# Optimization experiments

Hardware: AMD Instinct MI355X
Metric: run time of the kernel (lower is better)

Reference implementation:

```python
import jax, jax.numpy as jnp
import numpy as np

B, N, DIM = 2, 4096, 1024
QK = 128
HID = 2048  # int(2.0 * DIM)
EPS = 1e-5


def setup_inputs() -> dict:
    key = jax.random.key(0)
    ks = jax.random.split(key, 10)
    s = lambda fan_in: 1.0 / np.sqrt(fan_in)
    return {
        "x": jax.random.normal(ks[0], (B, N, DIM), dtype=jnp.float32),
        "ln_g": jnp.ones((DIM,), jnp.float32),
        "ln_b": jnp.zeros((DIM,), jnp.float32),
        "Wh": jax.random.uniform(ks[1], (DIM, 2 * HID), jnp.float32, -s(DIM), s(DIM)),
        "bh": jax.random.uniform(ks[2], (2 * HID,), jnp.float32, -s(DIM), s(DIM)),
        "Wqk": jax.random.uniform(ks[3], (DIM, QK), jnp.float32, -s(DIM), s(DIM)),
        "bqk": jax.random.uniform(ks[4], (QK,), jnp.float32, -s(DIM), s(DIM)),
        "gamma": 1.0 + 0.02 * jax.random.normal(ks[5], (2, QK), jnp.float32),
        "beta": jnp.zeros((2, QK), jnp.float32),
        "Wo": jax.random.uniform(ks[6], (HID, DIM), jnp.float32, -s(HID), s(HID)),
        "bo": jax.random.uniform(ks[7], (DIM,), jnp.float32, -s(HID), s(HID)),
    }


def _gau(x, ln_g, ln_b, Wh, bh, Wqk, bqk, gamma, beta, Wo, bo):
    n = x.shape[-2]
    # LayerNorm
    mu = jnp.mean(x, axis=-1, keepdims=True)
    var = jnp.var(x, axis=-1, keepdims=True)
    normed = (x - mu) * jax.lax.rsqrt(var + EPS) * ln_g + ln_b
    # hidden: v and gate
    hv = jax.nn.silu(normed @ Wh + bh)           # [b, n, 2*HID]
    v, gate = hv[..., :HID], hv[..., HID:]
    # q, k via shared projection + offset-scale (2 heads)
    qk = jax.nn.silu(normed @ Wqk + bqk)         # [b, n, QK]
    q = qk * gamma[0] + beta[0]
    k = qk * gamma[1] + beta[1]
    # ReLU^2 attention, scaled by 1/seq_len
    sim = jnp.einsum('bid,bjd->bij', q, k) / n   # [b, n, n]
    attn = jnp.square(jax.nn.relu(sim))
    # causal mask (zero out strict upper triangle)
    causal = jnp.tril(jnp.ones((n, n), dtype=bool))
    attn = jnp.where(causal, attn, 0.0)
    out = jnp.einsum('bij,bjd->bid', attn, v) * gate
    out = out @ Wo + bo
    return out + x  # residual


def reference(x, ln_g, ln_b, Wh, bh, Wqk, bqk, gamma, beta, Wo, bo):
    return _gau(x, ln_g, ln_b, Wh, bh, Wqk, bqk, gamma, beta, Wo, bo)
```

## Files before the change

kernel.cpp:

```cpp
#include <hip/hip_runtime.h>
#include <math.h>

typedef unsigned short u16;
typedef unsigned int u32;
typedef __attribute__((ext_vector_type(8))) __bf16 bf16x8;
typedef __attribute__((ext_vector_type(4))) float f32x4;

#define B_ 2
#define N_ 4096
#define DIM_ 1024
#define QK_ 128
#define HID_ 2048
#define M_TOT (B_*N_)

__device__ __forceinline__ u16 f2bf(float f) {
  union { float f; u32 u; } v; v.f = f;
  u32 r = v.u + 0x7fffu + ((v.u >> 16) & 1u);
  return (u16)(r >> 16);
}
__device__ __forceinline__ float bf2f(u16 h) {
  union { u32 u; float f; } v; v.u = ((u32)h) << 16;
  return v.f;
}
__device__ __forceinline__ float silu_f(float v) { return v / (1.0f + expf(-v)); }

#define WAIT_VM(n)  asm volatile("s_waitcnt vmcnt(" #n ")" ::: "memory")

__global__ __launch_bounds__(256) void ln_kernel(
    const float* __restrict__ x, const float* __restrict__ g,
    const float* __restrict__ b, u16* __restrict__ out) {
  const int row = blockIdx.x;
  const int t = threadIdx.x;
  const float4* xr = (const float4*)(x + (size_t)row * DIM_);
  float4 v = xr[t];
  float s  = v.x + v.y + v.z + v.w;
  float s2 = v.x*v.x + v.y*v.y + v.z*v.z + v.w*v.w;
  #pragma unroll
  for (int o = 32; o > 0; o >>= 1) { s += __shfl_down(s, o); s2 += __shfl_down(s2, o); }
  __shared__ float red[2][4];
  const int wave = t >> 6, lane = t & 63;
  if (lane == 0) { red[0][wave] = s; red[1][wave] = s2; }
  __syncthreads();
  float ts  = red[0][0] + red[0][1] + red[0][2] + red[0][3];
  float ts2 = red[1][0] + red[1][1] + red[1][2] + red[1][3];
  float mu  = ts * (1.0f/(float)DIM_);
  float var = ts2 * (1.0f/(float)DIM_) - mu*mu;
  float rs  = rsqrtf(var + 1e-5f);
  const float4 gg = ((const float4*)g)[t];
  const float4 bb = ((const float4*)b)[t];
  ushort4 w;
  w.x = f2bf((v.x-mu)*rs*gg.x + bb.x);
  w.y = f2bf((v.y-mu)*rs*gg.y + bb.y);
  w.z = f2bf((v.z-mu)*rs*gg.z + bb.z);
  w.w = f2bf((v.w-mu)*rs*gg.w + bb.w);
  ((ushort4*)(out + (size_t)row*DIM_))[t] = w;
}

__global__ __launch_bounds__(256) void transpose_k(
    const float* __restrict__ in, u16* __restrict__ out, int R, int C) {
  __shared__ float tile[32][33];
  const int c0 = blockIdx.x * 32, r0 = blockIdx.y * 32;
  const int tx = threadIdx.x & 31, ty = threadIdx.x >> 5;
  #pragma unroll
  for (int i = 0; i < 4; ++i)
    tile[ty + i*8][tx] = in[(size_t)(r0 + ty + i*8) * C + c0 + tx];
  __syncthreads();
  #pragma unroll
  for (int i = 0; i < 4; ++i)
    out[(size_t)(c0 + ty + i*8) * R + r0 + tx] = f2bf(tile[tx][ty + i*8]);
}

enum { EPI_HV, EPI_QK, EPI_S, EPI_PV, EPI_O };

template<int EPI>
__global__ __launch_bounds__(256, 4) void g2(
    const u16* __restrict__ A, int lda,
    const u16* __restrict__ BT, int ldb, int K,
    void* __restrict__ Cv, int ldc,
    const float* __restrict__ f0,
    const u16* __restrict__ gateT, const float* __restrict__ xres)
{
  int bm, bn; const int bz = blockIdx.z;
  if constexpr (EPI == EPI_HV) {
    const int id  = (int)blockIdx.x + 32*(int)blockIdx.y;
    const int nid = (id & 7)*256 + (id >> 3);
    bm = nid & 31; bn = nid >> 5;
  } else if constexpr (EPI == EPI_O) {
    const int id  = (int)blockIdx.x + 64*(int)blockIdx.y;
    const int nid = (id & 7)*64 + (id >> 3);
    bm = nid & 63; bn = nid >> 6;
  } else if constexpr (EPI == EPI_PV) {
    bn = blockIdx.x;
    bm = bz ? ((int)gridDim.y - 1 - (int)blockIdx.y) : (int)blockIdx.y;
  } else {
    bn = blockIdx.x; bm = blockIdx.y;
    if (bm < bn) return;
  }

  const u16* Ap = A; const u16* Bp = BT;
  if constexpr (EPI == EPI_S)  { Ap += (size_t)bz*N_*QK_; Bp += (size_t)bz*N_*QK_; }
  if constexpr (EPI == EPI_PV) { Ap += (size_t)bz*N_*N_;  Bp += (size_t)bz*N_; }

  __shared__ __align__(16) u16 lds[2][128*64];
  const int tid = threadIdx.x, wave = tid >> 6, lane = tid & 63;
  const int m0 = bm*128, n0 = bn*128;
  int kmax = K;
  if constexpr (EPI == EPI_PV) kmax = (bm+1)*128;
  f32x4 acc[4][4] = {};
  const int wr = (wave >> 1)*64, wc = (wave & 1)*64;

  const int srow = lane >> 3;
  const int sch  = (lane & 7) ^ srow;
  const u16* ga = Ap + (size_t)(m0 + srow)*lda + sch*8;
  const u16* gb = Bp + (size_t)(n0 + srow)*ldb + sch*8;

  const int l15   = lane & 15;
  const int cswz0 = ((((lane>>4)    ) ^ (lane&7)) << 3);
  const int cswz1 = ((((lane>>4) | 4) ^ (lane&7)) << 3);

  for (int k0 = 0; k0 < kmax; k0 += 64) {
    #pragma unroll
    for (int t = 0; t < 4; ++t) {
      const int chunk = wave*4 + t;
      __builtin_amdgcn_global_load_lds(
          (const __attribute__((address_space(1))) void*)(ga + (size_t)(chunk*8)*lda + k0),
          (__attribute__((address_space(3))) void*)&lds[0][chunk*512], 16, 0, 0);
      __builtin_amdgcn_global_load_lds(
          (const __attribute__((address_space(1))) void*)(gb + (size_t)(chunk*8)*ldb + k0),
          (__attribute__((address_space(3))) void*)&lds[1][chunk*512], 16, 0, 0);
    }
    __syncthreads();
    #pragma unroll
    for (int kk = 0; kk < 2; ++kk) {
      const int cs = kk ? cswz1 : cswz0;
      bf16x8 af[4], bfr[4];
      #pragma unroll
      for (int i = 0; i < 4; ++i) {
        af[i]  = *(const bf16x8*)&lds[0][(wr + i*16 + l15)*64 + cs];
        bfr[i] = *(const bf16x8*)&lds[1][(wc + i*16 + l15)*64 + cs];
      }
      #pragma unroll
      for (int i = 0; i < 4; ++i)
        #pragma unroll
        for (int j = 0; j < 4; ++j)
          acc[i][j] = __builtin_amdgcn_mfma_f32_16x16x32_bf16(af[i], bfr[j], acc[i][j], 0, 0, 0);
    }
    __syncthreads();
  }

  const int er = (lane >> 4)*4;
  #pragma unroll
  for (int i = 0; i < 4; ++i) {
    #pragma unroll
    for (int j = 0; j < 4; ++j) {
      #pragma unroll
      for (int e = 0; e < 4; ++e) {
        const int row = m0 + wr + i*16 + er + e;
        const int col = n0 + wc + j*16 + l15;
        float v = acc[i][j][e];
        if constexpr (EPI == EPI_HV) {
          ((u16*)Cv)[(size_t)row*ldc + col] = f2bf(silu_f(v + f0[row]));
        } else if constexpr (EPI == EPI_S) {
          float p = (row >= col && v > 0.0f) ? v*v : 0.0f;
          ((u16*)Cv)[(size_t)bz*N_*N_ + (size_t)row*ldc + col] = f2bf(p);
        } else if constexpr (EPI == EPI_PV) {
          float gate = bf2f(gateT[(size_t)(HID_ + col)*M_TOT + (size_t)bz*N_ + row]);
          ((u16*)Cv)[((size_t)bz*N_ + row)*ldc + col] = f2bf(v * gate);
        } else {
          ((float*)Cv)[(size_t)row*ldc + col] = v + f0[col] + xres[(size_t)row*DIM_ + col];
        }
      }
    }
  }
}

template<int BM, int EPI>
__global__ __launch_bounds__(256, 2) void ring4(
    const u16* __restrict__ A, int lda,
    const u16* __restrict__ BT, int ldb, int K,
    void* __restrict__ Cv, void* __restrict__ C2v, int ldc,
    const float* __restrict__ f0, const float* __restrict__ f1,
    const float* __restrict__ f2)
{
  constexpr int FRM  = BM/32;
  constexpr int LA   = BM/64;
  constexpr int ASZ  = BM*32;
  constexpr int SLOT = ASZ + 128*32;
  __shared__ __align__(16) u16 lds[4*SLOT];

  const int bm = blockIdx.x, bn = blockIdx.y;
  const int tid = threadIdx.x, wave = tid >> 6, lane = tid & 63;
  const int wm = wave >> 1, wn = wave & 1;
  const int m0 = bm*BM, n0 = bn*128;
  const int nt = K >> 5;

  f32x4 acc[FRM][4] = {};
  const int srow = lane >> 2;
  const int sq   = (lane & 3) ^ ((srow >> 1) & 3);

  auto stage = [&](int t) {
    if (t >= nt) return;
    const int k0 = t << 5;
    u16* sA = &lds[(t & 3) * SLOT];
    u16* sB = sA + ASZ;
    #pragma unroll
    for (int c = 0; c < LA; ++c) {
      const int ch = wave*LA + c;
      const u16* src = A + (size_t)(m0 + ch*16 + srow)*lda + k0 + sq*8;
      __builtin_amdgcn_global_load_lds(
          (const __attribute__((address_space(1))) void*)src,
          (__attribute__((address_space(3))) void*)(sA + ch*512), 16, 0, 0);
    }
    #pragma unroll
    for (int c = 0; c < 2; ++c) {
      const int ch = wave*2 + c;
      const u16* src = BT + (size_t)(n0 + ch*16 + srow)*ldb + k0 + sq*8;
      __builtin_amdgcn_global_load_lds(
          (const __attribute__((address_space(1))) void*)src,
          (__attribute__((address_space(3))) void*)(sB + ch*512), 16, 0, 0);
    }
  };

  stage(0); stage(1); stage(2);

  const int l15 = lane & 15;
  const int swz = (((lane >> 4) ^ ((l15 >> 1) & 3)) << 3);
  const int rA0 = (wm*(BM/2) + l15)*32;
  const int rB0 = (wn*64 + l15)*32;

  for (int t = 0; t < nt; ++t) {
    if (t + 2 < nt)      { WAIT_VM(8); }
    else if (t + 1 < nt) { WAIT_VM(4); }
    else                 { WAIT_VM(0); }
    __builtin_amdgcn_s_barrier();
    stage(t + 3);

    const u16* sA = &lds[(t & 3) * SLOT];
    const u16* sB = sA + ASZ;
    bf16x8 a_[FRM], b_[4];
    #pragma unroll
    for (int j = 0; j < 4; ++j) b_[j] = *(const bf16x8*)&sB[rB0 + j*512 + swz];
    #pragma unroll
    for (int i = 0; i < FRM; ++i) a_[i] = *(const bf16x8*)&sA[rA0 + i*512 + swz];
    #pragma unroll
    for (int i = 0; i < FRM; ++i)
      #pragma unroll
      for (int j = 0; j < 4; ++j)
        acc[i][j] = __builtin_amdgcn_mfma_f32_16x16x32_bf16(a_[i], b_[j], acc[i][j], 0, 0, 0);
  }

  const int er = (lane >> 4)*4;
  #pragma unroll
  for (int fi = 0; fi < FRM; ++fi) {
    #pragma unroll
    for (int fj = 0; fj < 4; ++fj) {
      #pragma unroll
      for (int e = 0; e < 4; ++e) {
        const int row = m0 + wm*(BM/2) + fi*16 + er + e;
        const int col = n0 + wn*64 + fj*16 + l15;
        float v = acc[fi][fj][e];
        if constexpr (EPI == EPI_QK) {
          float s = silu_f(v + f0[col]);
          float q = (s*f1[col]     + f2[col])     * (1.0f/(float)N_);
          float k2 = s*f1[QK_+col] + f2[QK_+col];
          ((u16*)Cv )[(size_t)row*ldc + col] = f2bf(q);
          ((u16*)C2v)[(size_t)row*ldc + col] = f2bf(k2);
        }
      }
    }
  }
}

extern "C" void kernel_launch(void* const* d_in, const int* in_sizes, int n_in,
                              void* d_out, int out_size, void* d_ws, size_t ws_size,
                              hipStream_t stream) {
  const float* x    = (const float*)d_in[0];
  const float* ln_g = (const float*)d_in[1];
  const float* ln_b = (const float*)d_in[2];
  const float* Wh   = (const float*)d_in[3];
  const float* bh   = (const float*)d_in[4];
  const float* Wqk  = (const float*)d_in[5];
  const float* bqk  = (const float*)d_in[6];
  const float* gamma= (const float*)d_in[7];
  const float* beta = (const float*)d_in[8];
  const float* Wo   = (const float*)d_in[9];
  const float* bo   = (const float*)d_in[10];
  float* out = (float*)d_out;
  char* ws = (char*)d_ws;

  u16* normed = (u16*)(ws + 0);
  u16* WhT    = (u16*)(ws + 16777216);
  u16* WqkT   = (u16*)(ws + 25165824);
  u16* WoT    = (u16*)(ws + 25427968);
  u16* hvT    = (u16*)(ws + 29622272);
  u16* qs     = (u16*)(ws + 96731136);
  u16* kb     = (u16*)(ws + 98828288);
  u16* P      = (u16*)(ws + 100925440);
  u16* a2     = (u16*)(ws + 168034304);

  ln_kernel<<<M_TOT, 256, 0, stream>>>(x, ln_g, ln_b, normed);
  transpose_k<<<dim3(4096/32, 1024/32), 256, 0, stream>>>(Wh,  WhT,  1024, 4096);
  transpose_k<<<dim3( 128/32, 1024/32), 256, 0, stream>>>(Wqk, WqkT, 1024, 128);
  transpose_k<<<dim3(1024/32, 2048/32), 256, 0, stream>>>(Wo,  WoT,  2048, 1024);

  g2<EPI_HV><<<dim3(32, 64), 256, 0, stream>>>(WhT, 1024, normed, 1024, 1024,
      hvT, 8192, bh, nullptr, nullptr);
  ring4<64, EPI_QK><<<dim3(128, 1), 256, 0, stream>>>(normed, 1024, WqkT, 1024, 1024,
      qs, kb, 128, bqk, gamma, beta);
  g2<EPI_S><<<dim3(32, 32, 2), 256, 0, stream>>>(qs, 128, kb, 128, 128,
      P, 4096, nullptr, nullptr, nullptr);
  g2<EPI_PV><<<dim3(16, 32, 2), 256, 0, stream>>>(P, 4096, hvT, 8192, 4096,
      a2, 2048, nullptr, hvT, nullptr);
  g2<EPI_O><<<dim3(64, 8), 256, 0, stream>>>(a2, 2048, WoT, 2048, 2048,
      out, 1024, bo, nullptr, x);
}
```

Before: 284.6 us.

## Add 8-wave ping-pong pipelined GEMM kernel for HV, PV and output projections

```diff
diff --git a/kernel.cpp b/kernel.cpp
--- a/kernel.cpp
+++ b/kernel.cpp
@@ -25,6 +25,7 @@
 __device__ __forceinline__ float silu_f(float v) { return v / (1.0f + expf(-v)); }
 
 #define WAIT_VM(n)  asm volatile("s_waitcnt vmcnt(" #n ")" ::: "memory")
+#define WAIT_LG0()  asm volatile("s_waitcnt lgkmcnt(0)" ::: "memory")
 
 __global__ __launch_bounds__(256) void ln_kernel(
     const float* __restrict__ x, const float* __restrict__ g,
@@ -81,31 +82,15 @@
     const u16* __restrict__ gateT, const float* __restrict__ xres)
 {
   int bm, bn; const int bz = blockIdx.z;
-  if constexpr (EPI == EPI_HV) {
-    const int id  = (int)blockIdx.x + 32*(int)blockIdx.y;
-    const int nid = (id & 7)*256 + (id >> 3);
-    bm = nid & 31; bn = nid >> 5;
-  } else if constexpr (EPI == EPI_O) {
-    const int id  = (int)blockIdx.x + 64*(int)blockIdx.y;
-    const int nid = (id & 7)*64 + (id >> 3);
-    bm = nid & 63; bn = nid >> 6;
-  } else if constexpr (EPI == EPI_PV) {
-    bn = blockIdx.x;
-    bm = bz ? ((int)gridDim.y - 1 - (int)blockIdx.y) : (int)blockIdx.y;
-  } else {
-    bn = blockIdx.x; bm = blockIdx.y;
-    if (bm < bn) return;
-  }
+  bn = blockIdx.x; bm = blockIdx.y;
+  if constexpr (EPI == EPI_S) { if (bm < bn) return; }
 
   const u16* Ap = A; const u16* Bp = BT;
   if constexpr (EPI == EPI_S)  { Ap += (size_t)bz*N_*QK_; Bp += (size_t)bz*N_*QK_; }
-  if constexpr (EPI == EPI_PV) { Ap += (size_t)bz*N_*N_;  Bp += (size_t)bz*N_; }
 
   __shared__ __align__(16) u16 lds[2][128*64];
   const int tid = threadIdx.x, wave = tid >> 6, lane = tid & 63;
   const int m0 = bm*128, n0 = bn*128;
-  int kmax = K;
-  if constexpr (EPI == EPI_PV) kmax = (bm+1)*128;
   f32x4 acc[4][4] = {};
   const int wr = (wave >> 1)*64, wc = (wave & 1)*64;
 
@@ -118,7 +103,7 @@
   const int cswz0 = ((((lane>>4)    ) ^ (lane&7)) << 3);
   const int cswz1 = ((((lane>>4) | 4) ^ (lane&7)) << 3);
 
-  for (int k0 = 0; k0 < kmax; k0 += 64) {
+  for (int k0 = 0; k0 < K; k0 += 64) {
     #pragma unroll
     for (int t = 0; t < 4; ++t) {
       const int chunk = wave*4 + t;
@@ -158,11 +143,162 @@
         const int row = m0 + wr + i*16 + er + e;
         const int col = n0 + wc + j*16 + l15;
         float v = acc[i][j][e];
+        if constexpr (EPI == EPI_S) {
+          float p = (row >= col && v > 0.0f) ? v*v : 0.0f;
+          ((u16*)Cv)[(size_t)bz*N_*N_ + (size_t)row*ldc + col] = f2bf(p);
+        }
+      }
+    }
+  }
+}
+
+template<int BM, int EPI>
+__global__ __launch_bounds__(512, 2) void p8(
+    const u16* __restrict__ A, int lda,
+    const u16* __restrict__ BT, int ldb, int K,
+    void* __restrict__ Cv, int ldc,
+    const float* __restrict__ f0,
+    const u16* __restrict__ gateT, const float* __restrict__ xres)
+{
+  constexpr int FR  = BM/32;
+  constexpr int HF  = FR/2;
+  constexpr int ATL = BM*64;
+  constexpr int SLT = ATL + 256*64;
+  __shared__ __align__(16) u16 lds[2*SLT];
+
+  int bm, bn;
+  const int bz = blockIdx.z;
+  if constexpr (EPI == EPI_HV) {
+    const int id  = (int)blockIdx.x + 16*(int)blockIdx.y;
+    const int nid = (id & 7)*64 + (id >> 3);
+    bm = nid & 15; bn = nid >> 4;
+  } else if constexpr (EPI == EPI_PV) {
+    bn = blockIdx.x;
+    bm = bz ? ((int)gridDim.y - 1 - (int)blockIdx.y) : (int)blockIdx.y;
+  } else { bm = blockIdx.x; bn = blockIdx.y; }
+
+  const int tid = threadIdx.x, wave = tid >> 6, lane = tid & 63;
+  const int wm = wave >> 2, wn = wave & 3;
+  const int m0 = bm*BM, n0 = bn*256;
+  const u16* Ap = A; const u16* Bp = BT;
+  if constexpr (EPI == EPI_PV) { Ap += (size_t)bz*N_*N_; Bp += (size_t)bz*N_; }
+  int kmax = K;
+  if constexpr (EPI == EPI_PV) kmax = (bm+1)*BM;
+  const int nt = kmax >> 6;
+
+  const int l15  = lane & 15;
+  const int c0   = (((lane>>4)    ) ^ (lane&7)) << 3;
+  const int c1   = (((lane>>4) | 4) ^ (lane&7)) << 3;
+  const int srow = lane >> 3;
+  const int scol = ((lane&7) ^ (lane>>3)) << 3;
+
+  f32x4 acc[FR][4] = {};
+  bf16x8 af[HF][2], b0[2][2], b1[2][2];
+
+  auto stage = [&](int slot, int unit, int t) {
+    if (t >= nt) return;
+    const int k0 = t << 6;
+    if (unit == 0 || unit == 3) {
+      const int ih = (unit == 3) ? 1 : 0;
+      constexpr int LA = BM/128;
+      #pragma unroll
+      for (int l = 0; l < LA; ++l) {
+        const int pa = wave*LA + l;
+        const int row0 = (pa/(BM/32))*(BM/2) + ih*(BM/4) + (pa%(BM/32))*8;
+        __builtin_amdgcn_global_load_lds(
+          (const __attribute__((address_space(1))) void*)(Ap + (size_t)(m0+row0+srow)*lda + k0 + scol),
+          (__attribute__((address_space(3))) void*)&lds[slot*SLT + row0*64], 16, 0, 0);
+      }
+    } else {
+      const int jh = (unit == 2) ? 1 : 0;
+      #pragma unroll
+      for (int l = 0; l < 2; ++l) {
+        const int pb = wave*2 + l;
+        const int row0 = (pb>>2)*64 + jh*32 + (pb&3)*8;
+        __builtin_amdgcn_global_load_lds(
+          (const __attribute__((address_space(1))) void*)(Bp + (size_t)(n0+row0+srow)*ldb + k0 + scol),
+          (__attribute__((address_space(3))) void*)&lds[slot*SLT + ATL + row0*64], 16, 0, 0);
+      }
+    }
+  };
+  auto rdA = [&](int slot, int ih) {
+    #pragma unroll
+    for (int i = 0; i < HF; ++i) {
+      const int R = wm*(BM/2) + ih*(BM/4) + i*16 + l15;
+      af[i][0] = *(const bf16x8*)&lds[slot*SLT + R*64 + c0];
+      af[i][1] = *(const bf16x8*)&lds[slot*SLT + R*64 + c1];
+    }
+  };
+  auto rdB = [&](int slot, int jh, bf16x8 (&bb)[2][2]) {
+    #pragma unroll
+    for (int j = 0; j < 2; ++j) {
+      const int R = wn*64 + jh*32 + j*16 + l15;
+      bb[j][0] = *(const bf16x8*)&lds[slot*SLT + ATL + R*64 + c0];
+      bb[j][1] = *(const bf16x8*)&lds[slot*SLT + ATL + R*64 + c1];
+    }
+  };
+  auto mma = [&](int ih, int jh, bf16x8 (&bb)[2][2]) {
+    __builtin_amdgcn_s_setprio(1);
+    #pragma unroll
+    for (int i = 0; i < HF; ++i)
+      #pragma unroll
+      for (int j = 0; j < 2; ++j)
+        #pragma unroll
+        for (int kk = 0; kk < 2; ++kk)
+          acc[ih*HF+i][jh*2+j] = __builtin_amdgcn_mfma_f32_16x16x32_bf16(
+              af[i][kk], bb[j][kk], acc[ih*HF+i][jh*2+j], 0, 0, 0);
+    __builtin_amdgcn_s_setprio(0);
+  };
+
+  #define BAR()     __builtin_amdgcn_s_barrier()
+  #define PH_TAIL() { BAR(); WAIT_LG0(); }
+  #define LG8()     if constexpr (BM==256) { asm volatile("s_waitcnt lgkmcnt(8)" ::: "memory"); }
+
+  stage(0,0,0); stage(0,1,0); stage(0,2,0); stage(0,3,0);
+  if constexpr (BM==256) { WAIT_VM(4); } else { WAIT_VM(3); }
+  stage(1,0,1); stage(1,1,1); stage(1,2,1);
+  if constexpr (BM==256) { WAIT_VM(6); } else { WAIT_VM(5); }
+  BAR();
+
+  const int iters = nt >> 1;
+  for (int it = 0; it < iters; ++it) {
+    const int kt = it*2;
+    const bool last = (it == iters-1);
+    rdA(0,0); rdB(0,0,b0); stage(1,3,kt+1);
+    LG8();
+    PH_TAIL(); mma(0,0,b0); BAR();
+    rdB(0,1,b1); stage(0,0,kt+2);
+    PH_TAIL(); mma(0,1,b1); BAR();
+    rdA(0,1); stage(0,1,kt+2);
+    PH_TAIL(); mma(1,1,b1); BAR();
+    stage(0,2,kt+2);
+    if (last) { WAIT_VM(0); }
+    else if constexpr (BM==256) { WAIT_VM(6); } else { WAIT_VM(5); }
+    PH_TAIL(); mma(1,0,b0); BAR();
+    rdA(1,0); rdB(1,0,b0); stage(0,3,kt+2);
+    LG8();
+    PH_TAIL(); mma(0,0,b0); BAR();
+    rdB(1,1,b1); stage(1,0,kt+3);
+    PH_TAIL(); mma(0,1,b1); BAR();
+    rdA(1,1); stage(1,1,kt+3);
+    PH_TAIL(); mma(1,1,b1); BAR();
+    stage(1,2,kt+3);
+    if constexpr (BM==256) { WAIT_VM(6); } else { WAIT_VM(5); }
+    PH_TAIL(); mma(1,0,b0); BAR();
+  }
+
+  const int er = (lane >> 4)*4;
+  #pragma unroll
+  for (int fi = 0; fi < FR; ++fi) {
+    #pragma unroll
+    for (int fj = 0; fj < 4; ++fj) {
+      #pragma unroll
+      for (int e = 0; e < 4; ++e) {
+        const int row = m0 + wm*(BM/2) + fi*16 + er + e;
+        const int col = n0 + wn*64 + fj*16 + l15;
+        float v = acc[fi][fj][e];
         if constexpr (EPI == EPI_HV) {
           ((u16*)Cv)[(size_t)row*ldc + col] = f2bf(silu_f(v + f0[row]));
-        } else if constexpr (EPI == EPI_S) {
-          float p = (row >= col && v > 0.0f) ? v*v : 0.0f;
-          ((u16*)Cv)[(size_t)bz*N_*N_ + (size_t)row*ldc + col] = f2bf(p);
         } else if constexpr (EPI == EPI_PV) {
           float gate = bf2f(gateT[(size_t)(HID_ + col)*M_TOT + (size_t)bz*N_ + row]);
           ((u16*)Cv)[((size_t)bz*N_ + row)*ldc + col] = f2bf(v * gate);
@@ -172,6 +308,9 @@
       }
     }
   }
+  #undef BAR
+  #undef PH_TAIL
+  #undef LG8
 }
 
 template<int BM, int EPI>
@@ -303,14 +442,14 @@
   transpose_k<<<dim3( 128/32, 1024/32), 256, 0, stream>>>(Wqk, WqkT, 1024, 128);
   transpose_k<<<dim3(1024/32, 2048/32), 256, 0, stream>>>(Wo,  WoT,  2048, 1024);
 
-  g2<EPI_HV><<<dim3(32, 64), 256, 0, stream>>>(WhT, 1024, normed, 1024, 1024,
+  p8<256, EPI_HV><<<dim3(16, 32), 512, 0, stream>>>(WhT, 1024, normed, 1024, 1024,
       hvT, 8192, bh, nullptr, nullptr);
   ring4<64, EPI_QK><<<dim3(128, 1), 256, 0, stream>>>(normed, 1024, WqkT, 1024, 1024,
       qs, kb, 128, bqk, gamma, beta);
   g2<EPI_S><<<dim3(32, 32, 2), 256, 0, stream>>>(qs, 128, kb, 128, 128,
       P, 4096, nullptr, nullptr, nullptr);
-  g2<EPI_PV><<<dim3(16, 32, 2), 256, 0, stream>>>(P, 4096, hvT, 8192, 4096,
+  p8<128, EPI_PV><<<dim3(8, 32, 2), 512, 0, stream>>>(P, 4096, hvT, 8192, 4096,
       a2, 2048, nullptr, hvT, nullptr);
-  g2<EPI_O><<<dim3(64, 8), 256, 0, stream>>>(a2, 2048, WoT, 2048, 2048,
+  p8<128, EPI_O><<<dim3(64, 4), 512, 0, stream>>>(a2, 2048, WoT, 2048, 2048,
       out, 1024, bo, nullptr, x);
 }
```

Result: faster. 266.4 us (-6.4%).
